# Performance work log

Measured on AMD Instinct MI355X. Metric: run time of the kernel, lower is better.

Reference implementation:

```python
import jax, jax.numpy as jnp
import numpy as np

TEMPERATURE = 8.0

def _non_neg(x):
    # exp(x) for x<0, x+1 for x>=0 (non-negative feature map)
    return jnp.where(x < 0, jnp.exp(x), x + 1.0)

def setup_inputs() -> dict:
    key = jax.random.key(0)
    kq, kk, kv, km = jax.random.split(key, 4)
    B, H, S, D = 8, 16, 4096, 64
    q = jax.random.normal(kq, (B, H, S, D), dtype=jnp.float32)
    k = jax.random.normal(kk, (B, H, S, D), dtype=jnp.float32)
    v = jax.random.normal(kv, (B, H, S, D), dtype=jnp.float32)
    token_mask = jax.random.randint(km, (B, S), 0, 2).astype(bool)
    return {"q": q, "k": k, "v": v, "token_mask": token_mask}

def reference(q, k, v, token_mask):
    B, H, S, D = q.shape
    idx = jnp.arange(S, dtype=q.dtype)
    cos_vec = jnp.cos(jnp.pi / 2.0 / S * idx)[:, None]  # [S,1], broadcasts over D
    sin_vec = jnp.sin(jnp.pi / 2.0 / S * idx)[:, None]
    qf = _non_neg(q)
    kf = _non_neg(k)
    q_cos = qf * cos_vec
    q_sin = qf * sin_vec
    k_cos = kf * cos_vec
    k_sin = kf * sin_vec
    mask = token_mask[:, None, :, None].astype(q.dtype)  # [B,1,S,1]
    q_cos = q_cos * mask
    q_sin = q_sin * mask
    # global context: [B,H,D,Dv]
    k_cos_v = jnp.einsum('bhsd,bhse->bhde', k_cos, v)
    k_sin_v = jnp.einsum('bhsd,bhse->bhde', k_sin, v)
    values = (jnp.einsum('bhsd,bhde->bhse', q_cos, k_cos_v)
              + jnp.einsum('bhsd,bhde->bhse', q_sin, k_sin_v)) / TEMPERATURE
    return values
```

## Files before the change

kernel.cpp:

```cpp
#include <hip/hip_runtime.h>
#include <math.h>

#define Sn 4096
#define Dn 64
#define CW 3.834951969714103e-4f
#define P1S 34
#define LDSU (64 * P1S)

typedef __attribute__((ext_vector_type(8))) short short8;
typedef __attribute__((ext_vector_type(4))) float f32x4;

__device__ __forceinline__ unsigned int pack2(float lo, float hi) {
    unsigned int a = __float_as_uint(lo) + 0x8000u;
    unsigned int b = __float_as_uint(hi) + 0x8000u;
    return __builtin_amdgcn_perm(b, a, 0x07060302u);
}
__device__ __forceinline__ float nneg(float x) {
    return x < 0.f ? __expf(x) : x + 1.f;
}
__device__ __forceinline__ short8 ld_frag(const unsigned int* p) {
    uint2 a = *(const uint2*)p;
    uint2 b = *(const uint2*)(p + 2);
    union { unsigned int u[4]; short8 s; } r;
    r.u[0] = a.x; r.u[1] = a.y; r.u[2] = b.x; r.u[3] = b.y;
    return r.s;
}

__global__ __launch_bounds__(256) void k_init(float4* kv4, int* flag,
                                              const unsigned char* mask_raw) {
    int i = blockIdx.x * 256 + threadIdx.x;
    kv4[i] = make_float4(0.f, 0.f, 0.f, 0.f);
    if (blockIdx.x == 0) {
        __shared__ int s_any;
        if (threadIdx.x == 0) s_any = 0;
        __syncthreads();
        int any = 0;
        int base = threadIdx.x * 16;
        #pragma unroll
        for (int j = 0; j < 16; j++) {
            int idx = base + j;
            if ((idx & 3) && mask_raw[idx]) any = 1;
        }
        if (any) s_any = 1;
        __syncthreads();
        if (threadIdx.x == 0) *flag = s_any ? 0 : 1;
    }
}

__global__ __launch_bounds__(256) void k_phase1(const float* __restrict__ kk,
                                                const float* __restrict__ vv,
                                                float* __restrict__ kv) {
    __shared__ unsigned int lds[2 * 3 * LDSU];
    const int t    = threadIdx.x;
    const int bh   = blockIdx.x >> 3;
    const int sblk = (blockIdx.x & 7) << 9;
    const int c    = t & 15;
    const int rp   = t >> 4;
    const int lane = t & 63;
    const int w    = t >> 6;
    const int n    = lane & 15;
    const int q4   = lane >> 4;
    const float* kb = kk + (size_t)bh * (Sn * Dn);
    const float* vb = vv + (size_t)bh * (Sn * Dn);

    f32x4 accC[4], accS[4];
    #pragma unroll
    for (int i = 0; i < 4; i++) {
        accC[i] = (f32x4){0.f, 0.f, 0.f, 0.f};
        accS[i] = (f32x4){0.f, 0.f, 0.f, 0.f};
    }

    float4 pk[2][4], pv[2][4];
    {
        const float* kp = kb + (size_t)(sblk + rp * 4) * Dn + c * 4;
        const float* vp = vb + (size_t)(sblk + rp * 4) * Dn + c * 4;
        #pragma unroll
        for (int i = 0; i < 4; i++) {
            pk[0][i] = *(const float4*)(kp + i * Dn);
            pv[0][i] = *(const float4*)(vp + i * Dn);
        }
    }

    #pragma unroll
    for (int chunk = 0; chunk < 8; chunk++) {
        const int cur = chunk & 1, nxt = cur ^ 1;
        const int s0 = sblk + chunk * 64;
        unsigned int* bKc = lds + cur * (3 * LDSU);
        unsigned int* bKs = bKc + LDSU;
        unsigned int* bV  = bKs + LDSU;
        float cs[4], sn[4], fk[4][4], fv[4][4];
        #pragma unroll
        for (int i = 0; i < 4; i++) {
            __sincosf(CW * (float)(s0 + rp * 4 + i), &sn[i], &cs[i]);
            fk[i][0] = nneg(pk[cur][i].x); fk[i][1] = nneg(pk[cur][i].y);
            fk[i][2] = nneg(pk[cur][i].z); fk[i][3] = nneg(pk[cur][i].w);
            fv[i][0] = pv[cur][i].x; fv[i][1] = pv[cur][i].y;
            fv[i][2] = pv[cur][i].z; fv[i][3] = pv[cur][i].w;
        }
        #pragma unroll
        for (int j = 0; j < 4; j++) {
            int d = c * 4 + j;
            uint2 wc, wsn, wv;
            wc.x  = pack2(fk[0][j] * cs[0], fk[1][j] * cs[1]);
            wc.y  = pack2(fk[2][j] * cs[2], fk[3][j] * cs[3]);
            wsn.x = pack2(fk[0][j] * sn[0], fk[1][j] * sn[1]);
            wsn.y = pack2(fk[2][j] * sn[2], fk[3][j] * sn[3]);
            wv.x  = pack2(fv[0][j], fv[1][j]);
            wv.y  = pack2(fv[2][j], fv[3][j]);
            *(uint2*)&bKc[d * P1S + rp * 2] = wc;
            *(uint2*)&bKs[d * P1S + rp * 2] = wsn;
            *(uint2*)&bV [d * P1S + rp * 2] = wv;
        }
        __syncthreads();
        if (chunk < 7) {
            const float* kp = kb + (size_t)(s0 + 64 + rp * 4) * Dn + c * 4;
            const float* vp = vb + (size_t)(s0 + 64 + rp * 4) * Dn + c * 4;
            #pragma unroll
            for (int i = 0; i < 4; i++) {
                pk[nxt][i] = *(const float4*)(kp + i * Dn);
                pv[nxt][i] = *(const float4*)(vp + i * Dn);
            }
        }
        #pragma unroll
        for (int ks = 0; ks < 2; ks++) {
            short8 Bv = ld_frag(&bV[(w * 16 + n) * P1S + ks * 16 + q4 * 4]);
            #pragma unroll
            for (int dt = 0; dt < 4; dt++) {
                short8 Ac = ld_frag(&bKc[(dt * 16 + n) * P1S + ks * 16 + q4 * 4]);
                short8 As = ld_frag(&bKs[(dt * 16 + n) * P1S + ks * 16 + q4 * 4]);
                accC[dt] = __builtin_amdgcn_mfma_f32_16x16x32_bf16(Ac, Bv, accC[dt], 0, 0, 0);
                accS[dt] = __builtin_amdgcn_mfma_f32_16x16x32_bf16(As, Bv, accS[dt], 0, 0, 0);
            }
        }
    }
    float* base = kv + (size_t)bh * 2 * 4096;
    const int e = w * 16 + n;
    #pragma unroll
    for (int dt = 0; dt < 4; dt++) {
        #pragma unroll
        for (int r = 0; r < 4; r++) {
            int d = dt * 16 + q4 * 4 + r;
            atomicAdd(base +        d * 64 + e, accC[dt][r]);
            atomicAdd(base + 4096 + d * 64 + e, accS[dt][r]);
        }
    }
}

__global__ __launch_bounds__(256) void k_phase2(const float* __restrict__ qq,
                                                const void* __restrict__ mask_raw,
                                                const float* __restrict__ kv,
                                                const int* __restrict__ flag,
                                                float* __restrict__ out) {
    const int t    = threadIdx.x;
    const int bh   = blockIdx.x >> 4;
    const int sblk = (blockIdx.x & 15) << 8;
    const int b    = bh >> 4;
    const int lane = t & 63;
    const int w    = t >> 6;
    const int n    = lane & 15;
    const int q4   = lane >> 4;
    const int iflag = *flag;

    const float* kvb = kv + (size_t)bh * 8192;
    short8 Bc[4][2], Bs[4][2];
    #pragma unroll
    for (int et = 0; et < 4; et++) {
        const int e = et * 16 + n;
        #pragma unroll
        for (int ks = 0; ks < 2; ks++) {
            const int d0 = ks * 32 + q4 * 8;
            union { unsigned int u[4]; short8 s; } uc, us;
            #pragma unroll
            for (int jj = 0; jj < 4; jj++) {
                float c0 = kvb[(size_t)(d0 + 2 * jj)     * 64 + e];
                float c1 = kvb[(size_t)(d0 + 2 * jj + 1) * 64 + e];
                float s0 = kvb[4096 + (size_t)(d0 + 2 * jj)     * 64 + e];
                float s1 = kvb[4096 + (size_t)(d0 + 2 * jj + 1) * 64 + e];
                uc.u[jj] = pack2(c0, c1);
                us.u[jj] = pack2(s0, s1);
            }
            Bc[et][ks] = uc.s;
            Bs[et][ks] = us.s;
        }
    }

    const float* qb = qq + (size_t)bh * (Sn * Dn);
    float* ob       = out + (size_t)bh * (Sn * Dn);
    const unsigned char* m8 = (const unsigned char*)mask_raw;
    const int* m32          = (const int*)mask_raw;

    float4 pq[2][4];
    float  pmv[2];
    {
        int s_row = sblk + w * 16 + n;
        const float* qp = qb + (size_t)s_row * Dn + q4 * 8;
        pq[0][0] = *(const float4*)(qp);
        pq[0][1] = *(const float4*)(qp + 4);
        pq[0][2] = *(const float4*)(qp + 32);
        pq[0][3] = *(const float4*)(qp + 36);
        pmv[0] = iflag ? (m32[b * Sn + s_row] ? 1.f : 0.f)
                       : (m8 [b * Sn + s_row] ? 1.f : 0.f);
    }

    #pragma unroll
    for (int strip = 0; strip < 4; strip++) {
        const int cur = strip & 1, nxt = cur ^ 1;
        const int s_base = sblk + strip * 64 + w * 16;
        const int s_row  = s_base + n;
        float cs, snv;
        __sincosf(CW * (float)s_row, &snv, &cs);
        cs *= pmv[cur]; snv *= pmv[cur];
        float f[16];
        f[0]  = nneg(pq[cur][0].x); f[1]  = nneg(pq[cur][0].y);
        f[2]  = nneg(pq[cur][0].z); f[3]  = nneg(pq[cur][0].w);
        f[4]  = nneg(pq[cur][1].x); f[5]  = nneg(pq[cur][1].y);
        f[6]  = nneg(pq[cur][1].z); f[7]  = nneg(pq[cur][1].w);
        f[8]  = nneg(pq[cur][2].x); f[9]  = nneg(pq[cur][2].y);
        f[10] = nneg(pq[cur][2].z); f[11] = nneg(pq[cur][2].w);
        f[12] = nneg(pq[cur][3].x); f[13] = nneg(pq[cur][3].y);
        f[14] = nneg(pq[cur][3].z); f[15] = nneg(pq[cur][3].w);
        union { unsigned int u[4]; short8 s; } ac0, as0, ac1, as1;
        #pragma unroll
        for (int j = 0; j < 4; j++) {
            ac0.u[j] = pack2(f[2*j]     * cs,  f[2*j + 1]     * cs);
            as0.u[j] = pack2(f[2*j]     * snv, f[2*j + 1]     * snv);
            ac1.u[j] = pack2(f[8 + 2*j] * cs,  f[8 + 2*j + 1] * cs);
            as1.u[j] = pack2(f[8 + 2*j] * snv, f[8 + 2*j + 1] * snv);
        }
        if (strip < 3) {
            int s_row2 = sblk + (strip + 1) * 64 + w * 16 + n;
            const float* qp = qb + (size_t)s_row2 * Dn + q4 * 8;
            pq[nxt][0] = *(const float4*)(qp);
            pq[nxt][1] = *(const float4*)(qp + 4);
            pq[nxt][2] = *(const float4*)(qp + 32);
            pq[nxt][3] = *(const float4*)(qp + 36);
            pmv[nxt] = iflag ? (m32[b * Sn + s_row2] ? 1.f : 0.f)
                             : (m8 [b * Sn + s_row2] ? 1.f : 0.f);
        }
        f32x4 acc[4];
        #pragma unroll
        for (int et = 0; et < 4; et++) acc[et] = (f32x4){0.f, 0.f, 0.f, 0.f};
        #pragma unroll
        for (int et = 0; et < 4; et++) {
            acc[et] = __builtin_amdgcn_mfma_f32_16x16x32_bf16(ac0.s, Bc[et][0], acc[et], 0, 0, 0);
            acc[et] = __builtin_amdgcn_mfma_f32_16x16x32_bf16(ac1.s, Bc[et][1], acc[et], 0, 0, 0);
            acc[et] = __builtin_amdgcn_mfma_f32_16x16x32_bf16(as0.s, Bs[et][0], acc[et], 0, 0, 0);
            acc[et] = __builtin_amdgcn_mfma_f32_16x16x32_bf16(as1.s, Bs[et][1], acc[et], 0, 0, 0);
        }
        #pragma unroll
        for (int et = 0; et < 4; et++) {
            #pragma unroll
            for (int r = 0; r < 4; r++) {
                int row = q4 * 4 + r;
                ob[(size_t)(s_base + row) * 64 + et * 16 + n] = acc[et][r] * 0.125f;
            }
        }
    }
}

extern "C" void kernel_launch(void* const* d_in, const int* in_sizes, int n_in,
                              void* d_out, int out_size, void* d_ws, size_t ws_size,
                              hipStream_t stream) {
    const float* q = (const float*)d_in[0];
    const float* k = (const float*)d_in[1];
    const float* v = (const float*)d_in[2];
    const void* mask = d_in[3];
    int*   flag = (int*)d_ws;
    float* kv   = (float*)((char*)d_ws + 256);

    k_init  <<<1024, 256, 0, stream>>>((float4*)kv, flag, (const unsigned char*)mask);
    k_phase1<<<1024, 256, 0, stream>>>(k, v, kv);
    k_phase2<<<2048, 256, 0, stream>>>(q, mask, kv, flag, (float*)d_out);
}
```

Baseline: 421.9 us.

## Drop LDS staging in phase1 using 32x32 MFMA with direct register fragments

Phase1 stops staging K/V through shared memory. Each lane now loads its own bf16 MFMA fragments straight from global memory, and the kernel uses the 32x32x16 MFMA, computing per-row sin/cos via angle-addition from a small table. Both kernels remap blocks so bh is the fastest index, and phase2 now handles 512 rows per block across half as many blocks. Phase2 output uses nontemporal stores. This removes LDS traffic and barriers, but the scalar strided global loads (one float per lane per row) may coalesce less efficiently than the previous float4 loads.

```diff
diff --git a/kernel.cpp b/kernel.cpp
--- a/kernel.cpp
+++ b/kernel.cpp
@@ -4,11 +4,10 @@
 #define Sn 4096
 #define Dn 64
 #define CW 3.834951969714103e-4f
-#define P1S 34
-#define LDSU (64 * P1S)
-
-typedef __attribute__((ext_vector_type(8))) short short8;
-typedef __attribute__((ext_vector_type(4))) float f32x4;
+
+typedef __attribute__((ext_vector_type(8)))  short short8;
+typedef __attribute__((ext_vector_type(4)))  float f32x4;
+typedef __attribute__((ext_vector_type(16))) float f32x16;
 
 __device__ __forceinline__ unsigned int pack2(float lo, float hi) {
     unsigned int a = __float_as_uint(lo) + 0x8000u;
@@ -17,13 +16,6 @@
 }
 __device__ __forceinline__ float nneg(float x) {
     return x < 0.f ? __expf(x) : x + 1.f;
-}
-__device__ __forceinline__ short8 ld_frag(const unsigned int* p) {
-    uint2 a = *(const uint2*)p;
-    uint2 b = *(const uint2*)(p + 2);
-    union { unsigned int u[4]; short8 s; } r;
-    r.u[0] = a.x; r.u[1] = a.y; r.u[2] = b.x; r.u[3] = b.y;
-    return r.s;
 }
 
 __global__ __launch_bounds__(256) void k_init(float4* kv4, int* flag,
@@ -47,102 +39,77 @@
     }
 }
 
-__global__ __launch_bounds__(256) void k_phase1(const float* __restrict__ kk,
-                                                const float* __restrict__ vv,
-                                                float* __restrict__ kv) {
-    __shared__ unsigned int lds[2 * 3 * LDSU];
+__global__ __launch_bounds__(256, 4) void k_phase1(const float* __restrict__ kk,
+                                                   const float* __restrict__ vv,
+                                                   float* __restrict__ kv) {
     const int t    = threadIdx.x;
-    const int bh   = blockIdx.x >> 3;
-    const int sblk = (blockIdx.x & 7) << 9;
-    const int c    = t & 15;
-    const int rp   = t >> 4;
+    const int bh   = blockIdx.x & 127;
+    const int sblk = (blockIdx.x >> 7) << 9;
     const int lane = t & 63;
     const int w    = t >> 6;
-    const int n    = lane & 15;
-    const int q4   = lane >> 4;
-    const float* kb = kk + (size_t)bh * (Sn * Dn);
-    const float* vb = vv + (size_t)bh * (Sn * Dn);
-
-    f32x4 accC[4], accS[4];
-    #pragma unroll
-    for (int i = 0; i < 4; i++) {
-        accC[i] = (f32x4){0.f, 0.f, 0.f, 0.f};
-        accS[i] = (f32x4){0.f, 0.f, 0.f, 0.f};
-    }
-
-    float4 pk[2][4], pv[2][4];
-    {
-        const float* kp = kb + (size_t)(sblk + rp * 4) * Dn + c * 4;
-        const float* vp = vb + (size_t)(sblk + rp * 4) * Dn + c * 4;
-        #pragma unroll
-        for (int i = 0; i < 4; i++) {
-            pk[0][i] = *(const float4*)(kp + i * Dn);
-            pv[0][i] = *(const float4*)(vp + i * Dn);
-        }
-    }
-
-    #pragma unroll
-    for (int chunk = 0; chunk < 8; chunk++) {
-        const int cur = chunk & 1, nxt = cur ^ 1;
-        const int s0 = sblk + chunk * 64;
-        unsigned int* bKc = lds + cur * (3 * LDSU);
-        unsigned int* bKs = bKc + LDSU;
-        unsigned int* bV  = bKs + LDSU;
-        float cs[4], sn[4], fk[4][4], fv[4][4];
-        #pragma unroll
-        for (int i = 0; i < 4; i++) {
-            __sincosf(CW * (float)(s0 + rp * 4 + i), &sn[i], &cs[i]);
-            fk[i][0] = nneg(pk[cur][i].x); fk[i][1] = nneg(pk[cur][i].y);
-            fk[i][2] = nneg(pk[cur][i].z); fk[i][3] = nneg(pk[cur][i].w);
-            fv[i][0] = pv[cur][i].x; fv[i][1] = pv[cur][i].y;
-            fv[i][2] = pv[cur][i].z; fv[i][3] = pv[cur][i].w;
-        }
-        #pragma unroll
-        for (int j = 0; j < 4; j++) {
-            int d = c * 4 + j;
-            uint2 wc, wsn, wv;
-            wc.x  = pack2(fk[0][j] * cs[0], fk[1][j] * cs[1]);
-            wc.y  = pack2(fk[2][j] * cs[2], fk[3][j] * cs[3]);
-            wsn.x = pack2(fk[0][j] * sn[0], fk[1][j] * sn[1]);
-            wsn.y = pack2(fk[2][j] * sn[2], fk[3][j] * sn[3]);
-            wv.x  = pack2(fv[0][j], fv[1][j]);
-            wv.y  = pack2(fv[2][j], fv[3][j]);
-            *(uint2*)&bKc[d * P1S + rp * 2] = wc;
-            *(uint2*)&bKs[d * P1S + rp * 2] = wsn;
-            *(uint2*)&bV [d * P1S + rp * 2] = wv;
-        }
-        __syncthreads();
-        if (chunk < 7) {
-            const float* kp = kb + (size_t)(s0 + 64 + rp * 4) * Dn + c * 4;
-            const float* vp = vb + (size_t)(s0 + 64 + rp * 4) * Dn + c * 4;
+    const int m    = lane & 31;
+    const int sl   = lane >> 5;
+    const int dt   = w >> 1;
+    const int et   = w & 1;
+
+    const float* kp = kk + (size_t)bh * (Sn * Dn) + (size_t)(sblk + sl * 8) * Dn + dt * 32 + m;
+    const float* vp = vv + (size_t)bh * (Sn * Dn) + (size_t)(sblk + sl * 8) * Dn + et * 32 + m;
+
+    const float CJT[8] = {1.0f,            0.999999926466f, 0.999999705859f, 0.999999338182f,
+                          0.999998823452f, 0.999998161643f, 0.999997352766f, 0.999996396820f};
+    const float SJT[8] = {0.0f,            3.83495188e-4f,  7.66989641e-4f,  1.15048534e-3f,
+                          1.53398019e-3f,  1.91747478e-3f,  2.30096910e-3f,  2.68446310e-3f};
+
+    f32x16 accC, accS;
+    #pragma unroll
+    for (int i = 0; i < 16; i++) { accC[i] = 0.f; accS[i] = 0.f; }
+
+    float rk[2][8], rv[2][8];
+    #pragma unroll
+    for (int j = 0; j < 8; j++) {
+        rk[0][j] = kp[j * Dn];
+        rv[0][j] = vp[j * Dn];
+    }
+    const float sb0 = (float)(sblk + sl * 8);
+
+    #pragma unroll 2
+    for (int st = 0; st < 32; ++st) {
+        const int cur = st & 1, nxt = cur ^ 1;
+        if (st < 31) {
+            const float* kq = kp + (size_t)(st + 1) * (16 * Dn);
+            const float* vq = vp + (size_t)(st + 1) * (16 * Dn);
             #pragma unroll
-            for (int i = 0; i < 4; i++) {
-                pk[nxt][i] = *(const float4*)(kp + i * Dn);
-                pv[nxt][i] = *(const float4*)(vp + i * Dn);
+            for (int j = 0; j < 8; j++) {
+                rk[nxt][j] = kq[j * Dn];
+                rv[nxt][j] = vq[j * Dn];
             }
         }
-        #pragma unroll
-        for (int ks = 0; ks < 2; ks++) {
-            short8 Bv = ld_frag(&bV[(w * 16 + n) * P1S + ks * 16 + q4 * 4]);
-            #pragma unroll
-            for (int dt = 0; dt < 4; dt++) {
-                short8 Ac = ld_frag(&bKc[(dt * 16 + n) * P1S + ks * 16 + q4 * 4]);
-                short8 As = ld_frag(&bKs[(dt * 16 + n) * P1S + ks * 16 + q4 * 4]);
-                accC[dt] = __builtin_amdgcn_mfma_f32_16x16x32_bf16(Ac, Bv, accC[dt], 0, 0, 0);
-                accS[dt] = __builtin_amdgcn_mfma_f32_16x16x32_bf16(As, Bv, accS[dt], 0, 0, 0);
-            }
-        }
-    }
-    float* base = kv + (size_t)bh * 2 * 4096;
-    const int e = w * 16 + n;
-    #pragma unroll
-    for (int dt = 0; dt < 4; dt++) {
-        #pragma unroll
-        for (int r = 0; r < 4; r++) {
-            int d = dt * 16 + q4 * 4 + r;
-            atomicAdd(base +        d * 64 + e, accC[dt][r]);
-            atomicAdd(base + 4096 + d * 64 + e, accS[dt][r]);
-        }
+        float sa, ca;
+        __sincosf(CW * (sb0 + (float)(st * 16)), &sa, &ca);
+        union { unsigned int u[4]; short8 s; } Ac, As, Bv;
+        #pragma unroll
+        for (int jj = 0; jj < 4; jj++) {
+            const float c0 = ca * CJT[2*jj]     - sa * SJT[2*jj];
+            const float s0 = sa * CJT[2*jj]     + ca * SJT[2*jj];
+            const float c1 = ca * CJT[2*jj + 1] - sa * SJT[2*jj + 1];
+            const float s1 = sa * CJT[2*jj + 1] + ca * SJT[2*jj + 1];
+            const float f0 = nneg(rk[cur][2*jj]);
+            const float f1 = nneg(rk[cur][2*jj + 1]);
+            Ac.u[jj] = pack2(f0 * c0, f1 * c1);
+            As.u[jj] = pack2(f0 * s0, f1 * s1);
+            Bv.u[jj] = pack2(rv[cur][2*jj], rv[cur][2*jj + 1]);
+        }
+        accC = __builtin_amdgcn_mfma_f32_32x32x16_bf16(Ac.s, Bv.s, accC, 0, 0, 0);
+        accS = __builtin_amdgcn_mfma_f32_32x32x16_bf16(As.s, Bv.s, accS, 0, 0, 0);
+    }
+
+    float* base = kv + (size_t)bh * 8192;
+    const int e = et * 32 + m;
+    #pragma unroll
+    for (int r = 0; r < 16; ++r) {
+        const int d = dt * 32 + (r & 3) + 8 * (r >> 2) + 4 * sl;
+        atomicAdd(base +        d * 64 + e, accC[r]);
+        atomicAdd(base + 4096 + d * 64 + e, accS[r]);
     }
 }
 
@@ -152,8 +119,8 @@
                                                 const int* __restrict__ flag,
                                                 float* __restrict__ out) {
     const int t    = threadIdx.x;
-    const int bh   = blockIdx.x >> 4;
-    const int sblk = (blockIdx.x & 15) << 8;
+    const int bh   = blockIdx.x & 127;
+    const int sblk = (blockIdx.x >> 7) << 9;
     const int b    = bh >> 4;
     const int lane = t & 63;
     const int w    = t >> 6;
@@ -202,8 +169,8 @@
                        : (m8 [b * Sn + s_row] ? 1.f : 0.f);
     }
 
-    #pragma unroll
-    for (int strip = 0; strip < 4; strip++) {
+    #pragma unroll 2
+    for (int strip = 0; strip < 8; strip++) {
         const int cur = strip & 1, nxt = cur ^ 1;
         const int s_base = sblk + strip * 64 + w * 16;
         const int s_row  = s_base + n;
@@ -227,7 +194,7 @@
             ac1.u[j] = pack2(f[8 + 2*j] * cs,  f[8 + 2*j + 1] * cs);
             as1.u[j] = pack2(f[8 + 2*j] * snv, f[8 + 2*j + 1] * snv);
         }
-        if (strip < 3) {
+        if (strip < 7) {
             int s_row2 = sblk + (strip + 1) * 64 + w * 16 + n;
             const float* qp = qb + (size_t)s_row2 * Dn + q4 * 8;
             pq[nxt][0] = *(const float4*)(qp);
@@ -252,7 +219,8 @@
             #pragma unroll
             for (int r = 0; r < 4; r++) {
                 int row = q4 * 4 + r;
-                ob[(size_t)(s_base + row) * 64 + et * 16 + n] = acc[et][r] * 0.125f;
+                __builtin_nontemporal_store(acc[et][r] * 0.125f,
+                    ob + (size_t)(s_base + row) * 64 + et * 16 + n);
             }
         }
     }
@@ -270,5 +238,5 @@
 
     k_init  <<<1024, 256, 0, stream>>>((float4*)kv, flag, (const unsigned char*)mask);
     k_phase1<<<1024, 256, 0, stream>>>(k, v, kv);
-    k_phase2<<<2048, 256, 0, stream>>>(q, mask, kv, flag, (float*)d_out);
-}
+    k_phase2<<<1024, 256, 0, stream>>>(q, mask, kv, flag, (float*)d_out);
+}
```

After: 421.6 us. No clear change (-0.1%).
